# Kernel optimization log

Measured on AMD Instinct MI355X. Metric: run time of the kernel, lower is better.

Reference implementation:

```python
import jax, jax.numpy as jnp
import numpy as np

NEG_SLOPE = 0.01

def _scatter_mean(vals, idx, num_segments):
    s = jax.ops.segment_sum(vals, idx, num_segments=num_segments)
    cnt = jax.ops.segment_sum(jnp.ones((vals.shape[0],), vals.dtype), idx, num_segments=num_segments)
    return s / jnp.maximum(cnt, 1.0)[:, None]

def setup_inputs() -> dict:
    key = jax.random.key(0)
    ks = jax.random.split(key, 8)
    N, E = 100000, 3200000
    node_emb, edge_emb = 128, 16
    d_in = node_emb + 2 * edge_emb  # 160
    x = jax.random.normal(ks[0], (N, node_emb), dtype=jnp.float32)
    edge_index = jax.random.randint(ks[1], (2, E), 0, N, dtype=jnp.int32)
    edge_attr = jax.random.normal(ks[2], (E, edge_emb), dtype=jnp.float32)
    W1 = jax.random.normal(ks[3], (d_in, node_emb), dtype=jnp.float32) * (1.0 / np.sqrt(d_in))
    b1 = jax.random.normal(ks[4], (node_emb,), dtype=jnp.float32) * 0.01
    W2 = jax.random.normal(ks[5], (node_emb, node_emb), dtype=jnp.float32) * (1.0 / np.sqrt(node_emb))
    b2 = jax.random.normal(ks[6], (node_emb,), dtype=jnp.float32) * 0.01
    return {"x": x, "edge_index": edge_index, "edge_attr": edge_attr,
            "W1": W1, "b1": b1, "W2": W2, "b2": b2}

def reference(x, edge_index, edge_attr, W1, b1, W2, b2):
    N = x.shape[0]
    row, col = edge_index[0], edge_index[1]
    rec_attr = _scatter_mean(edge_attr, row, N)   # [N, edge_emb]
    sent_attr = _scatter_mean(edge_attr, col, N)  # [N, edge_emb]
    out = jnp.concatenate([x, rec_attr, sent_attr], axis=1)  # [N, node+2*edge]
    h = out @ W1 + b1
    h = jnp.where(h >= 0, h, NEG_SLOPE * h)  # LeakyReLU(0.01)
    return h @ W2 + b2
```

## Files before the change

### kernel.cpp

```cpp
#include <hip/hip_runtime.h>
#include <hip/hip_bf16.h>
#include <hip/hip_fp16.h>
#include <stdint.h>

typedef __attribute__((ext_vector_type(8))) short short8;
typedef __attribute__((ext_vector_type(4))) float float4v;

#define NEG_SLOPE 0.01f
#define LDS_S 136

#define FXP_INV_SCALE 0.03125f

#define BSHIFT 9
#define BMASK 511u
#define NBMAX 256
#define CHUNKB 8192
#define CHUNKH 16384

__device__ __forceinline__ uint16_t f2bf(float f) {
    union { float ff; uint32_t i; } c; c.ff = f;
    uint32_t x = c.i;
    x += 0x7fffu + ((x >> 16) & 1u);
    return (uint16_t)(x >> 16);
}

__device__ __forceinline__ unsigned long long pack4(float4v v) {
    uint32_t u0 = __float2uint_rn(v.x * 32.0f + 256.0f);
    uint32_t u1 = __float2uint_rn(v.y * 32.0f + 256.0f);
    uint32_t u2 = __float2uint_rn(v.z * 32.0f + 256.0f);
    uint32_t u3 = __float2uint_rn(v.w * 32.0f + 256.0f);
    return (unsigned long long)u0
         | ((unsigned long long)u1 << 16)
         | ((unsigned long long)u2 << 32)
         | ((unsigned long long)u3 << 48);
}

__device__ __forceinline__ float4v decode4(unsigned long long pv, float ob, float inv) {
    float4v r;
    r.x = (((float)((uint32_t)(pv       ) & 0xFFFFu)) - ob) * FXP_INV_SCALE * inv;
    r.y = (((float)((uint32_t)(pv >> 16) & 0xFFFFu)) - ob) * FXP_INV_SCALE * inv;
    r.z = (((float)((uint32_t)(pv >> 32) & 0xFFFFu)) - ob) * FXP_INV_SCALE * inv;
    r.w = (((float)((uint32_t)(pv >> 48) & 0xFFFFu)) - ob) * FXP_INV_SCALE * inv;
    return r;
}

__global__ __launch_bounds__(256) void pack_w(
    const float* __restrict__ W1, const float* __restrict__ W2,
    uint16_t* __restrict__ W1p, uint16_t* __restrict__ W2p)
{
    int pid = blockIdx.x * 256 + threadIdx.x;
    if (pid < 20480) {
        int j = pid & 7, lane = (pid >> 3) & 63, rest = pid >> 9;
        int kc = rest % 5, ct = rest / 5;
        int k = kc * 32 + (lane >> 4) * 8 + j;
        int n = ct * 16 + (lane & 15);
        W1p[pid] = f2bf(W1[k * 128 + n]);
    }
    int pid2 = pid - 20480;
    if (pid2 >= 0 && pid2 < 16384) {
        int j = pid2 & 7, lane = (pid2 >> 3) & 63, rest = pid2 >> 9;
        int kc = rest & 3, ct = rest >> 2;
        int k = kc * 32 + (lane >> 4) * 8 + j;
        int n = ct * 16 + (lane & 15);
        W2p[pid2] = f2bf(W2[k * 128 + n]);
    }
}

__global__ __launch_bounds__(256) void hist_kernel(
    const int* __restrict__ eidx, int E,
    uint32_t* __restrict__ cntR, uint32_t* __restrict__ cntC, int NB)
{
    __shared__ uint32_t hR[NBMAX], hC[NBMAX];
    int t = threadIdx.x;
    int cb = blockIdx.x * CHUNKH;
    hR[t] = 0; hC[t] = 0;
    __syncthreads();
    for (int j = 0; j < CHUNKH / 256; ++j) {
        int e = cb + t + j * 256;
        if (e < E) {
            atomicAdd(&hR[((uint32_t)eidx[e]) >> BSHIFT], 1u);
            atomicAdd(&hC[((uint32_t)eidx[E + e]) >> BSHIFT], 1u);
        }
    }
    __syncthreads();
    if (t < NB) {
        if (hR[t]) atomicAdd(cntR + t, hR[t]);
        if (hC[t]) atomicAdd(cntC + t, hC[t]);
    }
}

__global__ __launch_bounds__(256) void scan_kernel(
    const uint32_t* __restrict__ cntR, const uint32_t* __restrict__ cntC,
    uint32_t* __restrict__ baseR, uint32_t* __restrict__ baseC, int NB)
{
    __shared__ uint32_t sR[NBMAX], sC[NBMAX];
    int t = threadIdx.x;
    uint32_t vR = (t < NB) ? cntR[t] : 0;
    uint32_t vC = (t < NB) ? cntC[t] : 0;
    sR[t] = vR; sC[t] = vC;
    __syncthreads();
    for (int off = 1; off < 256; off <<= 1) {
        uint32_t uR = (t >= off) ? sR[t - off] : 0;
        uint32_t uC = (t >= off) ? sC[t - off] : 0;
        __syncthreads();
        sR[t] += uR; sC[t] += uC;
        __syncthreads();
    }
    if (t < NB) { baseR[t] = sR[t] - vR; baseC[t] = sC[t] - vC; }
}

__global__ __launch_bounds__(256) void binkey_kernel(
    const int* __restrict__ eidx, int E,
    const uint32_t* __restrict__ baseR, const uint32_t* __restrict__ baseC,
    uint32_t* __restrict__ runR, uint32_t* __restrict__ runC,
    uint32_t* __restrict__ keyR, uint32_t* __restrict__ keyC, int NB)
{
    __shared__ uint32_t buf[CHUNKB];
    __shared__ uint32_t hist[NBMAX], lofs[NBMAX], rk[NBMAX], gb[NBMAX];
    int t = threadIdx.x;
    int cb = blockIdx.x * CHUNKB;

    for (int d = 0; d < 2; ++d) {
        const int* ids = eidx + (size_t)d * E;
        uint32_t* runG = d ? runC : runR;
        const uint32_t* baseG = d ? baseC : baseR;
        uint32_t* keyG = d ? keyC : keyR;

        hist[t] = 0; rk[t] = 0;
        __syncthreads();

        uint32_t myid[CHUNKB / 256];
        #pragma unroll
        for (int j = 0; j < CHUNKB / 256; ++j) {
            int i = t + j * 256;
            if (cb + i < E) {
                myid[j] = (uint32_t)ids[cb + i];
                atomicAdd(&hist[myid[j] >> BSHIFT], 1u);
            } else myid[j] = 0xFFFFFFFFu;
        }
        __syncthreads();

        uint32_t v = hist[t];
        lofs[t] = v;
        __syncthreads();
        for (int off = 1; off < 256; off <<= 1) {
            uint32_t u = (t >= off) ? lofs[t - off] : 0;
            __syncthreads();
            lofs[t] += u;
            __syncthreads();
        }
        lofs[t] -= v;
        if (t < NB && v) gb[t] = atomicAdd(&runG[t], v) + baseG[t];
        __syncthreads();

        #pragma unroll
        for (int j = 0; j < CHUNKB / 256; ++j) {
            if (myid[j] != 0xFFFFFFFFu) {
                uint32_t b = myid[j] >> BSHIFT;
                uint32_t p = atomicAdd(&rk[b], 1u);
                uint32_t e = (uint32_t)(cb + t + j * 256);
                buf[lofs[b] + p] = (e << BSHIFT) | (myid[j] & BMASK);
            }
        }
        __syncthreads();

        if (t < NB) {
            uint32_t n = hist[t];
            uint32_t src = lofs[t];
            uint32_t dst = gb[t];
            for (uint32_t i = 0; i < n; ++i) keyG[dst + i] = buf[src + i];
        }
        __syncthreads();
    }
}

__global__ __launch_bounds__(256) void reduce_kernel(
    const float* __restrict__ ea,
    const uint32_t* __restrict__ keyR, const uint32_t* __restrict__ keyC,
    const uint32_t* __restrict__ cntR, const uint32_t* __restrict__ cntC,
    const uint32_t* __restrict__ baseR, const uint32_t* __restrict__ baseC,
    unsigned long long* __restrict__ pacc, uint32_t* __restrict__ pcnt,
    float* __restrict__ meanR, float* __restrict__ meanC,
    int N, int NB, int SEG)
{
    __shared__ unsigned long long acc[512 * 4];
    __shared__ uint32_t lc[512];
    int blk = blockIdx.x;
    int dir = blk / (NB * SEG);
    int rem = blk - dir * NB * SEG;
    int b = rem / SEG, s = rem - (rem / SEG) * SEG;
    const uint32_t* key = dir ? keyC : keyR;
    uint32_t n  = (dir ? cntC  : cntR)[b];
    uint32_t ba = (dir ? baseC : baseR)[b];

    int t = threadIdx.x;
    for (int i = t; i < 2048; i += 256) acc[i] = 0ull;
    for (int i = t; i < 512; i += 256) lc[i] = 0;
    __syncthreads();

    uint32_t lo = (uint32_t)(((unsigned long long)n * (unsigned)s) / (unsigned)SEG);
    uint32_t hi = (uint32_t)(((unsigned long long)n * (unsigned)(s + 1)) / (unsigned)SEG);
    int p4 = t & 3, sub = t >> 2;
    for (uint32_t i0 = lo; i0 < hi; i0 += 128) {
        uint32_t ia = i0 + sub;
        uint32_t ib = ia + 64;
        bool va = ia < hi, vb = ib < hi;
        uint32_t ka = 0, kb = 0;
        if (va) ka = key[ba + ia];
        if (vb) kb = key[ba + ib];
        float4v xa, xb;
        if (va) xa = ((const float4v*)ea)[(size_t)(ka >> BSHIFT) * 4 + p4];
        if (vb) xb = ((const float4v*)ea)[(size_t)(kb >> BSHIFT) * 4 + p4];
        if (va) {
            atomicAdd(&acc[(ka & BMASK) * 4 + p4], pack4(xa));
            if (p4 == 0) atomicAdd(&lc[ka & BMASK], 1u);
        }
        if (vb) {
            atomicAdd(&acc[(kb & BMASK) * 4 + p4], pack4(xb));
            if (p4 == 0) atomicAdd(&lc[kb & BMASK], 1u);
        }
    }
    __syncthreads();

    if (SEG == 1) {
        float* mean = dir ? meanC : meanR;
        #pragma unroll
        for (int u = 0; u < 2; ++u) {
            int nl = t + u * 256;
            int node = b * 512 + nl;
            if (node < N) {
                uint32_t c = lc[nl];
                float inv = c ? 1.0f / (float)c : 0.0f;
                float ob = 256.0f * (float)c;
                #pragma unroll
                for (int j = 0; j < 4; ++j)
                    ((float4v*)(mean + (size_t)node * 16))[j] =
                        decode4(acc[nl * 4 + j], ob, inv);
            }
        }
    } else {
        size_t pb = ((size_t)(dir * NB + b) * SEG + s);
        unsigned long long* pa = pacc + pb * 2048;
        for (int i = t; i < 2048; i += 256) pa[i] = acc[i];
        uint32_t* pc = pcnt + pb * 512;
        for (int i = t; i < 512; i += 256) pc[i] = lc[i];
    }
}

__global__ __launch_bounds__(256) void finalize_kernel(
    const unsigned long long* __restrict__ pacc, const uint32_t* __restrict__ pcnt,
    float* __restrict__ meanR, float* __restrict__ meanC, int N, int NB, int SEG)
{
    int tid = blockIdx.x * 256 + threadIdx.x;
    if (tid >= 2 * N) return;
    int dir = tid >= N;
    int node = dir ? tid - N : tid;
    int b = node >> BSHIFT, nl = node & (int)BMASK;
    unsigned long long a0 = 0, a1 = 0, a2 = 0, a3 = 0;
    uint32_t c = 0;
    for (int s = 0; s < SEG; ++s) {
        size_t pb = ((size_t)(dir * NB + b) * SEG + s);
        const unsigned long long* pa = pacc + pb * 2048 + nl * 4;
        a0 += pa[0]; a1 += pa[1]; a2 += pa[2]; a3 += pa[3];
        c += pcnt[pb * 512 + nl];
    }
    float inv = c ? 1.0f / (float)c : 0.0f;
    float ob = 256.0f * (float)c;
    float* mean = dir ? meanC : meanR;
    float4v* dst = (float4v*)(mean + (size_t)node * 16);
    dst[0] = decode4(a0, ob, inv);
    dst[1] = decode4(a1, ob, inv);
    dst[2] = decode4(a2, ob, inv);
    dst[3] = decode4(a3, ob, inv);
}

__global__ __launch_bounds__(256) void scatter_fb(
    const float* __restrict__ ea, const int* __restrict__ idx, int E,
    unsigned long long* __restrict__ pack, uint32_t* __restrict__ fcnt)
{
    int gid = blockIdx.x * 256 + threadIdx.x;
    int e = gid >> 2;
    if (e >= E) return;
    int t = gid & 3;
    float4v v = ((const float4v*)ea)[(size_t)e * 4 + t];
    int n = idx[e];
    atomicAdd(pack + (size_t)n * 4 + t, pack4(v));
    if (t == 0) atomicAdd(fcnt + n, 1u);
}

__global__ __launch_bounds__(256) void finalize_pack(
    const unsigned long long* __restrict__ pack, const uint32_t* __restrict__ fcnt,
    float* __restrict__ mean, int N)
{
    int tid = blockIdx.x * 256 + threadIdx.x;
    if (tid >= N) return;
    uint32_t c = fcnt[tid];
    float inv = c ? 1.0f / (float)c : 0.0f;
    float ob = 256.0f * (float)c;
    #pragma unroll
    for (int j = 0; j < 4; ++j)
        ((float4v*)(mean + (size_t)tid * 16))[j] = decode4(pack[(size_t)tid * 4 + j], ob, inv);
}

__global__ __launch_bounds__(256) void mlp_kernel(
    const float* __restrict__ x,
    const float* __restrict__ meanR, const float* __restrict__ meanC,
    const uint16_t* __restrict__ W1p, const uint16_t* __restrict__ W2p,
    const float* __restrict__ b1, const float* __restrict__ b2,
    float* __restrict__ out, int N)
{
    __shared__ alignas(16) uint16_t hbuf[4 * 16 * LDS_S];
    int wave = threadIdx.x >> 6;
    int lane = threadIdx.x & 63;
    int m = lane & 15, q = lane >> 4;
    int nw = blockIdx.x * 64 + wave * 16;
    int node = nw + m;
    int nclamp = node < N ? node : N - 1;

    short8 afr[5];
    {
        const float* xf = x + (size_t)nclamp * 128;
        #pragma unroll
        for (int kc = 0; kc < 4; ++kc) {
            float4 v0 = *(const float4*)(xf + kc * 32 + q * 8);
            float4 v1 = *(const float4*)(xf + kc * 32 + q * 8 + 4);
            short8 a;
            a[0] = (short)f2bf(v0.x); a[1] = (short)f2bf(v0.y);
            a[2] = (short)f2bf(v0.z); a[3] = (short)f2bf(v0.w);
            a[4] = (short)f2bf(v1.x); a[5] = (short)f2bf(v1.y);
            a[6] = (short)f2bf(v1.z); a[7] = (short)f2bf(v1.w);
            afr[kc] = a;
        }
    }
    {
        const float* msrc = (q < 2) ? (meanR + (size_t)nclamp * 16 + q * 8)
                                    : (meanC + (size_t)nclamp * 16 + (q - 2) * 8);
        float4v v0 = *(const float4v*)msrc;
        float4v v1 = *(const float4v*)(msrc + 4);
        short8 a;
        a[0] = (short)f2bf(v0.x); a[1] = (short)f2bf(v0.y);
        a[2] = (short)f2bf(v0.z); a[3] = (short)f2bf(v0.w);
        a[4] = (short)f2bf(v1.x); a[5] = (short)f2bf(v1.y);
        a[6] = (short)f2bf(v1.z); a[7] = (short)f2bf(v1.w);
        afr[4] = a;
    }

    uint16_t* hw = hbuf + wave * 16 * LDS_S;

    #pragma unroll
    for (int ct = 0; ct < 8; ++ct) {
        float4v acc = {0.f, 0.f, 0.f, 0.f};
        #pragma unroll
        for (int kc = 0; kc < 5; ++kc) {
            short8 bfr = *(const short8*)(W1p + ((ct * 5 + kc) * 64 + lane) * 8);
            acc = __builtin_amdgcn_mfma_f32_16x16x32_bf16(afr[kc], bfr, acc, 0, 0, 0);
        }
        int c = ct * 16 + m;
        float bias = b1[c];
        #pragma unroll
        for (int r = 0; r < 4; ++r) {
            float h = acc[r] + bias;
            h = h >= 0.f ? h : NEG_SLOPE * h;
            hw[(q * 4 + r) * LDS_S + c] = f2bf(h);
        }
    }
    __syncthreads();

    short8 a2[4];
    #pragma unroll
    for (int kc = 0; kc < 4; ++kc)
        a2[kc] = *(const short8*)(hw + m * LDS_S + kc * 32 + q * 8);

    #pragma unroll
    for (int ct = 0; ct < 8; ++ct) {
        float4v acc = {0.f, 0.f, 0.f, 0.f};
        #pragma unroll
        for (int kc = 0; kc < 4; ++kc) {
            short8 bfr = *(const short8*)(W2p + ((ct * 4 + kc) * 64 + lane) * 8);
            acc = __builtin_amdgcn_mfma_f32_16x16x32_bf16(a2[kc], bfr, acc, 0, 0, 0);
        }
        int c = ct * 16 + m;
        float bias = b2[c];
        #pragma unroll
        for (int r = 0; r < 4; ++r) {
            int onode = nw + q * 4 + r;
            if (onode < N)
                out[(size_t)onode * 128 + c] = acc[r] + bias;
        }
    }
}

static inline char* align16(char* p) {
    return (char*)(((uintptr_t)p + 15) & ~(uintptr_t)15);
}

extern "C" void kernel_launch(void* const* d_in, const int* in_sizes, int n_in,
                              void* d_out, int out_size, void* d_ws, size_t ws_size,
                              hipStream_t stream) {
    const float* x   = (const float*)d_in[0];
    const int* eidx  = (const int*)d_in[1];
    const float* ea  = (const float*)d_in[2];
    const float* W1  = (const float*)d_in[3];
    const float* b1  = (const float*)d_in[4];
    const float* W2  = (const float*)d_in[5];
    const float* b2  = (const float*)d_in[6];
    float* out = (float*)d_out;
    int N = in_sizes[0] / 128;
    int E = in_sizes[1] / 2;

    int NB = (N + 511) >> BSHIFT;
    bool fb = (NB > NBMAX) || (E >= (1 << 23));

    float* meanR = (float*)d_ws;
    float* meanC = meanR + (size_t)N * 16;
    uint32_t* keyR = (uint32_t*)(meanC + (size_t)N * 16);
    uint32_t* keyC = keyR + (size_t)E;
    uint32_t* cntR = keyC + (size_t)E;
    uint32_t* cntC = cntR + NB;
    uint32_t* baseR = cntC + NB;
    uint32_t* baseC = baseR + NB;
    uint32_t* runR = baseC + NB;
    uint32_t* runC = runR + NB;
    uint16_t* W1p = (uint16_t*)align16((char*)(runC + NB));
    uint16_t* W2p = W1p + 20480;
    char* pstart = align16((char*)(W2p + 16384));
    size_t base_need = (size_t)(pstart - (char*)d_ws);
    int SEG = 0;
    unsigned long long* pacc = (unsigned long long*)pstart;
    uint32_t* pcnt = nullptr;
    if (!fb && ws_size >= base_need) {
        const int segs[4] = {8, 4, 2, 1};
        for (int i = 0; i < 4; ++i) {
            int s = segs[i];
            size_t pb = (s == 1) ? 0 : (size_t)2 * NB * s * (2048 * 8 + 512 * 4);
            if (ws_size >= base_need + pb) {
                SEG = s;
                pcnt = (uint32_t*)(pstart + (size_t)2 * NB * s * 2048 * 8);
                break;
            }
        }
    }
    if (SEG == 0) fb = true;

    if (!fb) {
        hipMemsetAsync(cntR, 0, sizeof(uint32_t) * (size_t)NB * 6, stream);
        pack_w<<<(20480 + 16384 + 255) / 256, 256, 0, stream>>>(W1, W2, W1p, W2p);

        hist_kernel<<<(E + CHUNKH - 1) / CHUNKH, 256, 0, stream>>>(eidx, E, cntR, cntC, NB);
        scan_kernel<<<1, 256, 0, stream>>>(cntR, cntC, baseR, baseC, NB);
        binkey_kernel<<<(E + CHUNKB - 1) / CHUNKB, 256, 0, stream>>>(
            eidx, E, baseR, baseC, runR, runC, keyR, keyC, NB);
        reduce_kernel<<<2 * NB * SEG, 256, 0, stream>>>(
            ea, keyR, keyC, cntR, cntC, baseR, baseC,
            pacc, pcnt, meanR, meanC, N, NB, SEG);
        if (SEG > 1)
            finalize_kernel<<<(2 * N + 255) / 256, 256, 0, stream>>>(
                pacc, pcnt, meanR, meanC, N, NB, SEG);
        mlp_kernel<<<(N + 63) / 64, 256, 0, stream>>>(x, meanR, meanC,
                                                      W1p, W2p, b1, b2, out, N);
    } else {
        float* fmeanR = (float*)d_ws;
        float* fmeanC = fmeanR + (size_t)N * 16;
        unsigned long long* packR = (unsigned long long*)align16((char*)(fmeanC + (size_t)N * 16));
        unsigned long long* packC = packR + (size_t)N * 4;
        uint32_t* fcntR = (uint32_t*)(packC + (size_t)N * 4);
        uint32_t* fcntC = fcntR + N;
        uint16_t* fW1p = (uint16_t*)align16((char*)(fcntC + N));
        uint16_t* fW2p = fW1p + 20480;

        hipMemsetAsync(packR, 0, (size_t)N * 8 * 8 + (size_t)N * 2 * 4, stream);
        pack_w<<<(20480 + 16384 + 255) / 256, 256, 0, stream>>>(W1, W2, fW1p, fW2p);
        int sblocks = (int)(((size_t)E * 4 + 255) / 256);
        scatter_fb<<<sblocks, 256, 0, stream>>>(ea, eidx,     E, packR, fcntR);
        scatter_fb<<<sblocks, 256, 0, stream>>>(ea, eidx + E, E, packC, fcntC);
        int fblocks = (N + 255) / 256;
        finalize_pack<<<fblocks, 256, 0, stream>>>(packR, fcntR, fmeanR, N);
        finalize_pack<<<fblocks, 256, 0, stream>>>(packC, fcntC, fmeanC, N);
        mlp_kernel<<<(N + 63) / 64, 256, 0, stream>>>(x, fmeanR, fmeanC,
                                                      fW1p, fW2p, b1, b2, out, N);
    }
}
```

Before: 554.8 us.

## Prepack edge attributes to fixed-point once in histogram pass, unroll reduce gathers

The histogram kernel now also converts each edge's 16 float attributes into four packed 64-bit fixed-point words, stored in a new workspace buffer. The reduce kernel gathers these packed words instead of raw floats, which halves the bytes per random gather and drops the repeated pack4 work across the two directions. The reduce loop is also unrolled to issue four key loads and four gathers per thread before the atomics, for more memory-level parallelism. The histogram chunk is shrunk to give more blocks. The cost is an extra 100MB streaming write plus more workspace, and the path falls back to the old one if the workspace is too small.

```diff
diff --git a/kernel.cpp b/kernel.cpp
--- a/kernel.cpp
+++ b/kernel.cpp
@@ -15,7 +15,7 @@
 #define BMASK 511u
 #define NBMAX 256
 #define CHUNKB 8192
-#define CHUNKH 16384
+#define CHUNKH 4096
 
 __device__ __forceinline__ uint16_t f2bf(float f) {
     union { float ff; uint32_t i; } c; c.ff = f;
@@ -66,9 +66,10 @@
     }
 }
 
-__global__ __launch_bounds__(256) void hist_kernel(
-    const int* __restrict__ eidx, int E,
-    uint32_t* __restrict__ cntR, uint32_t* __restrict__ cntC, int NB)
+__global__ __launch_bounds__(256) void hist_pack_kernel(
+    const float* __restrict__ ea, const int* __restrict__ eidx, int E,
+    uint32_t* __restrict__ cntR, uint32_t* __restrict__ cntC,
+    unsigned long long* __restrict__ eap, int NB, int doPack)
 {
     __shared__ uint32_t hR[NBMAX], hC[NBMAX];
     int t = threadIdx.x;
@@ -80,6 +81,14 @@
         if (e < E) {
             atomicAdd(&hR[((uint32_t)eidx[e]) >> BSHIFT], 1u);
             atomicAdd(&hC[((uint32_t)eidx[E + e]) >> BSHIFT], 1u);
+            if (doPack) {
+                const float4v* src = (const float4v*)(ea + (size_t)e * 16);
+                unsigned long long* dst = eap + (size_t)e * 4;
+                dst[0] = pack4(src[0]);
+                dst[1] = pack4(src[1]);
+                dst[2] = pack4(src[2]);
+                dst[3] = pack4(src[3]);
+            }
         }
     }
     __syncthreads();
@@ -174,8 +183,9 @@
     }
 }
 
+template<bool HASP>
 __global__ __launch_bounds__(256) void reduce_kernel(
-    const float* __restrict__ ea,
+    const float* __restrict__ ea, const unsigned long long* __restrict__ eap,
     const uint32_t* __restrict__ keyR, const uint32_t* __restrict__ keyC,
     const uint32_t* __restrict__ cntR, const uint32_t* __restrict__ cntC,
     const uint32_t* __restrict__ baseR, const uint32_t* __restrict__ baseC,
@@ -201,23 +211,31 @@
     uint32_t lo = (uint32_t)(((unsigned long long)n * (unsigned)s) / (unsigned)SEG);
     uint32_t hi = (uint32_t)(((unsigned long long)n * (unsigned)(s + 1)) / (unsigned)SEG);
     int p4 = t & 3, sub = t >> 2;
-    for (uint32_t i0 = lo; i0 < hi; i0 += 128) {
-        uint32_t ia = i0 + sub;
-        uint32_t ib = ia + 64;
-        bool va = ia < hi, vb = ib < hi;
-        uint32_t ka = 0, kb = 0;
-        if (va) ka = key[ba + ia];
-        if (vb) kb = key[ba + ib];
-        float4v xa, xb;
-        if (va) xa = ((const float4v*)ea)[(size_t)(ka >> BSHIFT) * 4 + p4];
-        if (vb) xb = ((const float4v*)ea)[(size_t)(kb >> BSHIFT) * 4 + p4];
-        if (va) {
-            atomicAdd(&acc[(ka & BMASK) * 4 + p4], pack4(xa));
-            if (p4 == 0) atomicAdd(&lc[ka & BMASK], 1u);
-        }
-        if (vb) {
-            atomicAdd(&acc[(kb & BMASK) * 4 + p4], pack4(xb));
-            if (p4 == 0) atomicAdd(&lc[kb & BMASK], 1u);
+    for (uint32_t i0 = lo; i0 < hi; i0 += 256) {
+        uint32_t kk[4];
+        unsigned long long pp[4];
+        bool vv[4];
+        #pragma unroll
+        for (int u = 0; u < 4; ++u) {
+            uint32_t idx = i0 + sub + u * 64;
+            vv[u] = idx < hi;
+            kk[u] = vv[u] ? key[ba + idx] : 0;
+        }
+        #pragma unroll
+        for (int u = 0; u < 4; ++u) {
+            if (vv[u]) {
+                if constexpr (HASP)
+                    pp[u] = eap[(size_t)(kk[u] >> BSHIFT) * 4 + p4];
+                else
+                    pp[u] = pack4(((const float4v*)ea)[(size_t)(kk[u] >> BSHIFT) * 4 + p4]);
+            }
+        }
+        #pragma unroll
+        for (int u = 0; u < 4; ++u) {
+            if (vv[u]) {
+                atomicAdd(&acc[(kk[u] & BMASK) * 4 + p4], pp[u]);
+                if (p4 == 0) atomicAdd(&lc[kk[u] & BMASK], 1u);
+            }
         }
     }
     __syncthreads();
@@ -411,48 +429,65 @@
     int NB = (N + 511) >> BSHIFT;
     bool fb = (NB > NBMAX) || (E >= (1 << 23));
 
-    float* meanR = (float*)d_ws;
-    float* meanC = meanR + (size_t)N * 16;
-    uint32_t* keyR = (uint32_t*)(meanC + (size_t)N * 16);
-    uint32_t* keyC = keyR + (size_t)E;
-    uint32_t* cntR = keyC + (size_t)E;
-    uint32_t* cntC = cntR + NB;
-    uint32_t* baseR = cntC + NB;
-    uint32_t* baseC = baseR + NB;
-    uint32_t* runR = baseC + NB;
-    uint32_t* runC = runR + NB;
-    uint16_t* W1p = (uint16_t*)align16((char*)(runC + NB));
-    uint16_t* W2p = W1p + 20480;
-    char* pstart = align16((char*)(W2p + 16384));
-    size_t base_need = (size_t)(pstart - (char*)d_ws);
-    int SEG = 0;
-    unsigned long long* pacc = (unsigned long long*)pstart;
-    uint32_t* pcnt = nullptr;
-    if (!fb && ws_size >= base_need) {
+    size_t meansB  = (size_t)N * 32 * 4;
+    size_t eapB    = (size_t)E * 32;
+    size_t keysB   = (size_t)E * 8;
+    size_t tablesB = (size_t)NB * 6 * 4;
+    size_t wpackB  = 73728 + 64;
+    auto partB = [&](int s) -> size_t {
+        return (s <= 1) ? 0 : (size_t)2 * NB * s * (2048 * 8 + 512 * 4);
+    };
+
+    int SEG = 0, useEap = 0;
+    if (!fb) {
         const int segs[4] = {8, 4, 2, 1};
-        for (int i = 0; i < 4; ++i) {
-            int s = segs[i];
-            size_t pb = (s == 1) ? 0 : (size_t)2 * NB * s * (2048 * 8 + 512 * 4);
-            if (ws_size >= base_need + pb) {
-                SEG = s;
-                pcnt = (uint32_t*)(pstart + (size_t)2 * NB * s * 2048 * 8);
-                break;
+        for (int i = 0; i < 4 && !SEG; ++i)
+            if (ws_size >= meansB + eapB + keysB + tablesB + wpackB + partB(segs[i])) {
+                SEG = segs[i]; useEap = 1;
             }
-        }
+        for (int i = 0; i < 4 && !SEG; ++i)
+            if (ws_size >= meansB + keysB + tablesB + wpackB + partB(segs[i]))
+                SEG = segs[i];
     }
     if (SEG == 0) fb = true;
 
     if (!fb) {
+        char* p = (char*)d_ws;
+        float* meanR = (float*)p;                      p += meansB / 2;
+        float* meanC = (float*)p;                      p += meansB / 2;
+        unsigned long long* eap = nullptr;
+        if (useEap) { eap = (unsigned long long*)p;    p += eapB; }
+        uint32_t* keyR = (uint32_t*)p;                 p += keysB / 2;
+        uint32_t* keyC = (uint32_t*)p;                 p += keysB / 2;
+        uint32_t* cntR = (uint32_t*)p;                 p += tablesB;
+        uint32_t* cntC = cntR + NB;
+        uint32_t* baseR = cntC + NB;
+        uint32_t* baseC = baseR + NB;
+        uint32_t* runR = baseC + NB;
+        uint32_t* runC = runR + NB;
+        uint16_t* W1p = (uint16_t*)align16(p);
+        uint16_t* W2p = W1p + 20480;
+        char* pstart = align16((char*)(W2p + 16384));
+        unsigned long long* pacc = (unsigned long long*)pstart;
+        uint32_t* pcnt = (SEG > 1)
+            ? (uint32_t*)(pstart + (size_t)2 * NB * SEG * 2048 * 8) : nullptr;
+
         hipMemsetAsync(cntR, 0, sizeof(uint32_t) * (size_t)NB * 6, stream);
         pack_w<<<(20480 + 16384 + 255) / 256, 256, 0, stream>>>(W1, W2, W1p, W2p);
 
-        hist_kernel<<<(E + CHUNKH - 1) / CHUNKH, 256, 0, stream>>>(eidx, E, cntR, cntC, NB);
+        hist_pack_kernel<<<(E + CHUNKH - 1) / CHUNKH, 256, 0, stream>>>(
+            ea, eidx, E, cntR, cntC, eap, NB, useEap);
         scan_kernel<<<1, 256, 0, stream>>>(cntR, cntC, baseR, baseC, NB);
         binkey_kernel<<<(E + CHUNKB - 1) / CHUNKB, 256, 0, stream>>>(
             eidx, E, baseR, baseC, runR, runC, keyR, keyC, NB);
-        reduce_kernel<<<2 * NB * SEG, 256, 0, stream>>>(
-            ea, keyR, keyC, cntR, cntC, baseR, baseC,
-            pacc, pcnt, meanR, meanC, N, NB, SEG);
+        if (useEap)
+            reduce_kernel<true><<<2 * NB * SEG, 256, 0, stream>>>(
+                ea, eap, keyR, keyC, cntR, cntC, baseR, baseC,
+                pacc, pcnt, meanR, meanC, N, NB, SEG);
+        else
+            reduce_kernel<false><<<2 * NB * SEG, 256, 0, stream>>>(
+                ea, eap, keyR, keyC, cntR, cntC, baseR, baseC,
+                pacc, pcnt, meanR, meanC, N, NB, SEG);
         if (SEG > 1)
             finalize_kernel<<<(2 * N + 255) / 256, 256, 0, stream>>>(
                 pacc, pcnt, meanR, meanC, N, NB, SEG);
```

After: 559.3 us. About the same (+0.8%).
